# Kernel tuning notes

Measured on AMD Instinct MI355X. Metric: run time of the kernel, lower is better.

The kernel has to match this reference:

```python
import jax, jax.numpy as jnp
import numpy as np

LN_EPS = 1e-3  # keras LayerNormalization default epsilon


def setup_inputs() -> dict:
    key = jax.random.key(0)
    ks = jax.random.split(key, 6)
    B, H, W, C = 8, 64, 64, 256
    s = 1.0 / np.sqrt(C)
    return {
        "x": jax.random.normal(ks[0], (B, H, W, C), jnp.float32),
        "gamma": jnp.ones((C,), jnp.float32),
        "beta": jnp.zeros((C,), jnp.float32),
        "wq": jax.random.normal(ks[1], (C, C), jnp.float32) * s,
        "bq": jnp.zeros((C,), jnp.float32),
        "wk": jax.random.normal(ks[2], (C, C), jnp.float32) * s,
        "bk": jnp.zeros((C,), jnp.float32),
        "wv": jax.random.normal(ks[3], (C, C), jnp.float32) * s,
        "bv": jnp.zeros((C,), jnp.float32),
        "wo": jax.random.normal(ks[4], (C, C), jnp.float32) * s,
        "bo": jnp.zeros((C,), jnp.float32),
    }


def reference(x, gamma, beta, wq, bq, wk, bk, wv, bv, wo, bo):
    B, H, W, C = x.shape
    # LayerNormalization over channel axis (keras default axis=-1, eps=1e-3)
    mean = jnp.mean(x, axis=-1, keepdims=True)
    var = jnp.mean(jnp.square(x - mean), axis=-1, keepdims=True)
    h = (x - mean) * jax.lax.rsqrt(var + LN_EPS) * gamma + beta

    q = h @ wq + bq
    k = h @ wk + bk
    v = h @ wv + bv

    # flatten spatial dims: single-head attention over N = H*W positions
    N = H * W
    qf = q.reshape(B, N, C)
    kf = k.reshape(B, N, C)
    vf = v.reshape(B, N, C)

    scale = jnp.asarray(C, x.dtype) ** -0.5
    scores = jnp.einsum('bnc,bmc->bnm', qf, kf) * scale  # [B, N, N]
    attn = jax.nn.softmax(scores, axis=-1)
    o = jnp.einsum('bnm,bmc->bnc', attn, vf).reshape(B, H, W, C)

    o = o @ wo + bo
    return x + o
```

## Files before the change

### kernel.cpp

```cpp
#include <hip/hip_runtime.h>
#include <hip/hip_bf16.h>
#include <stdint.h>

typedef __attribute__((ext_vector_type(8))) short bf16x8;
typedef __attribute__((ext_vector_type(4))) short s16x4;
typedef __attribute__((ext_vector_type(4))) float f32x4;

__device__ __forceinline__ unsigned short f2b(float x) {
  __hip_bfloat16 h = __float2bfloat16(x);
  unsigned short u;
  __builtin_memcpy(&u, &h, 2);
  return u;
}

__device__ __forceinline__ float b2f(unsigned short u) {
  unsigned v = (unsigned)u << 16;
  float f;
  __builtin_memcpy(&f, &v, 4);
  return f;
}

__device__ __forceinline__ void glds16(const void* g, void* l) {
  __builtin_amdgcn_global_load_lds((const __attribute__((address_space(1))) void*)g,
                                   (__attribute__((address_space(3))) void*)l,
                                   16, 0, 0);
}

__device__ __forceinline__ float wred_add(float v) {
#pragma unroll
  for (int o = 32; o >= 1; o >>= 1) v += __shfl_xor(v, o, 64);
  return v;
}

__global__ __launch_bounds__(256) void gemm_qkv(
    const unsigned short* __restrict__ h, const unsigned short* __restrict__ wT,
    const float* __restrict__ bq, const float* __restrict__ bk, const float* __restrict__ bv,
    unsigned short* __restrict__ q, unsigned short* __restrict__ kk,
    unsigned short* __restrict__ vT, float qscale)
{
  __shared__ unsigned short As[128 * 32];
  __shared__ unsigned short Bs[128 * 32];
  const int t = threadIdx.x;
  const int lane = t & 63;
  const int wv_ = t >> 6;
  const int wr = wv_ >> 1, wc = wv_ & 1;
  const int z = blockIdx.z;
  const long long row0 = (long long)blockIdx.y * 128;
  const int col0 = blockIdx.x * 128;
  const unsigned short* Bt = wT + z * 65536;
  const float* bias = z == 0 ? bq : z == 1 ? bk : bv;
  const float scale = z == 0 ? qscale : 1.0f;

  const int sr = t >> 2;
  const int sc = (t & 3) * 8;
  const unsigned short* ga = h + (row0 + sr) * 256 + sc;
  const unsigned short* gb = Bt + (col0 + sr) * 256 + sc;
  char* lA = (char*)As + (t >> 6) * 1024;
  char* lB = (char*)Bs + (t >> 6) * 1024;

  const int l15 = lane & 15;
  const int l4 = lane >> 4;
  const unsigned short* pa = As + (wr * 64 + l15) * 32 + l4 * 8;
  const unsigned short* pb = Bs + (wc * 64 + l15) * 32 + l4 * 8;

  f32x4 acc[4][4] = {};

  for (int k0 = 0; k0 < 256; k0 += 32) {
    glds16(ga, lA);
    glds16(ga + 64 * 256, lA + 4096);
    glds16(gb, lB);
    glds16(gb + 64 * 256, lB + 4096);
    ga += 32;
    gb += 32;
    __syncthreads();
    bf16x8 a[4], b[4];
#pragma unroll
    for (int i = 0; i < 4; i++) a[i] = *(const bf16x8*)(pa + i * 512);
#pragma unroll
    for (int j = 0; j < 4; j++) b[j] = *(const bf16x8*)(pb + j * 512);
#pragma unroll
    for (int i = 0; i < 4; i++)
#pragma unroll
      for (int j = 0; j < 4; j++)
        acc[i][j] = __builtin_amdgcn_mfma_f32_16x16x32_bf16(a[i], b[j], acc[i][j], 0, 0, 0);
    __syncthreads();
  }

#pragma unroll
  for (int i = 0; i < 4; i++) {
#pragma unroll
    for (int j = 0; j < 4; j++) {
      const int col = col0 + wc * 64 + j * 16 + l15;
      const float bv_ = bias[col];
#pragma unroll
      for (int r = 0; r < 4; r++) {
        const long long row = row0 + wr * 64 + i * 16 + l4 * 4 + r;
        const float val = (acc[i][j][r] + bv_) * scale;
        if (z == 0) {
          q[row * 256 + col] = f2b(val);
        } else if (z == 1) {
          kk[row * 256 + col] = f2b(val);
        } else {
          const int bb = (int)(row >> 12), rr = (int)(row & 4095);
          const int kl = rr & 31;
          const int rrp = (rr & ~31) | ((((kl >> 2) & 3) << 3) | (((kl >> 4) & 1) << 2) | (kl & 3));
          vT[((long long)bb * 256 + col) * 4096 + rrp] = f2b(val);
        }
      }
    }
  }
}

__global__ __launch_bounds__(256) void gemm_out(
    const unsigned short* __restrict__ A, const unsigned short* __restrict__ Bt,
    float* __restrict__ C, const float* __restrict__ bias,
    const float* __restrict__ resid)
{
  __shared__ unsigned short As[128 * 32];
  __shared__ unsigned short Bs[128 * 32];
  const int t = threadIdx.x;
  const int lane = t & 63;
  const int wv_ = t >> 6;
  const int wr = wv_ >> 1, wc = wv_ & 1;
  const long long row0 = (long long)blockIdx.y * 128;
  const int col0 = blockIdx.x * 128;

  const int sr = t >> 2;
  const int sc = (t & 3) * 8;
  const unsigned short* ga = A + (row0 + sr) * 256 + sc;
  const unsigned short* gb = Bt + (col0 + sr) * 256 + sc;
  char* lA = (char*)As + (t >> 6) * 1024;
  char* lB = (char*)Bs + (t >> 6) * 1024;

  const int l15 = lane & 15;
  const int l4 = lane >> 4;
  const unsigned short* pa = As + (wr * 64 + l15) * 32 + l4 * 8;
  const unsigned short* pb = Bs + (wc * 64 + l15) * 32 + l4 * 8;

  f32x4 acc[4][4] = {};

  for (int k0 = 0; k0 < 256; k0 += 32) {
    glds16(ga, lA);
    glds16(ga + 64 * 256, lA + 4096);
    glds16(gb, lB);
    glds16(gb + 64 * 256, lB + 4096);
    ga += 32;
    gb += 32;
    __syncthreads();
    bf16x8 a[4], b[4];
#pragma unroll
    for (int i = 0; i < 4; i++) a[i] = *(const bf16x8*)(pa + i * 512);
#pragma unroll
    for (int j = 0; j < 4; j++) b[j] = *(const bf16x8*)(pb + j * 512);
#pragma unroll
    for (int i = 0; i < 4; i++)
#pragma unroll
      for (int j = 0; j < 4; j++)
        acc[i][j] = __builtin_amdgcn_mfma_f32_16x16x32_bf16(a[i], b[j], acc[i][j], 0, 0, 0);
    __syncthreads();
  }

#pragma unroll
  for (int i = 0; i < 4; i++) {
#pragma unroll
    for (int j = 0; j < 4; j++) {
      const int col = col0 + wc * 64 + j * 16 + l15;
      const float bv_ = bias[col];
#pragma unroll
      for (int r = 0; r < 4; r++) {
        const long long row = row0 + wr * 64 + i * 16 + l4 * 4 + r;
        const long long idx = row * 256 + col;
        C[idx] = resid[idx] + acc[i][j][r] + bv_;
      }
    }
  }
}

__global__ __launch_bounds__(512) void ln_bf16(const float* __restrict__ x,
                                               const float* __restrict__ gamma,
                                               const float* __restrict__ beta,
                                               unsigned short* __restrict__ h)
{
  const int w = threadIdx.x >> 6;
  const int lane = threadIdx.x & 63;
  const long long row = (long long)blockIdx.x * 8 + w;
  const f32x4 v = *(const f32x4*)(x + row * 256 + lane * 4);
  const f32x4 g = *(const f32x4*)(gamma + lane * 4);
  const f32x4 be = *(const f32x4*)(beta + lane * 4);
  float s = v[0] + v[1] + v[2] + v[3];
  float s2 = v[0] * v[0] + v[1] * v[1] + v[2] * v[2] + v[3] * v[3];
#pragma unroll
  for (int o = 32; o >= 1; o >>= 1) {
    s += __shfl_xor(s, o, 64);
    s2 += __shfl_xor(s2, o, 64);
  }
  const float mean = s * (1.f / 256.f);
  const float var = s2 * (1.f / 256.f) - mean * mean;
  const float rstd = rsqrtf(var + 1e-3f);
  s16x4 out;
#pragma unroll
  for (int e = 0; e < 4; e++) out[e] = (short)f2b((v[e] - mean) * rstd * g[e] + be[e]);
  *(s16x4*)(h + row * 256 + lane * 4) = out;
}

__global__ void wtrans(const float* __restrict__ wq, const float* __restrict__ wk,
                       const float* __restrict__ wv, const float* __restrict__ wo,
                       unsigned short* __restrict__ wT)
{
  const float* w = blockIdx.z == 0 ? wq : blockIdx.z == 1 ? wk : blockIdx.z == 2 ? wv : wo;
  unsigned short* o = wT + (long long)blockIdx.z * 65536;
  __shared__ float tile[16][17];
  const int tx = threadIdx.x, ty = threadIdx.y;
  const int bx = blockIdx.x * 16, by = blockIdx.y * 16;
  tile[ty][tx] = w[(by + ty) * 256 + bx + tx];
  __syncthreads();
  o[(bx + ty) * 256 + (by + tx)] = f2b(tile[tx][ty]);
}

#define FL_LDS (64 * 1024)

__global__ __launch_bounds__(256, 2) void flash(
    const unsigned short* __restrict__ q,
    const unsigned short* __restrict__ kk,
    const unsigned short* __restrict__ vT,
    unsigned short* __restrict__ o0,
    unsigned short* __restrict__ o1,
    float2* __restrict__ ml0,
    float2* __restrict__ ml1)
{
  extern __shared__ char lds[];
  const int t = threadIdx.x;
  const int w = t >> 6;
  const int lane = t & 63;
  const int l15 = lane & 15, hi = lane >> 4;
  const int b = blockIdx.x & 7;
  const int kh = (blockIdx.x >> 3) & 1;
  const int qb = blockIdx.x >> 4;
  const long long qrow = (long long)b * 4096 + (long long)qb * 128 + w * 32;

  const unsigned short* kbase = kk + (long long)b * 4096 * 256 + (long long)kh * 2048 * 256;
  const unsigned short* vbase = vT + (long long)b * 256 * 4096 + kh * 2048;

  const int gs_k = (t & 31) ^ ((t >> 5) & 7);
  const unsigned short* Kst = kbase + (t >> 5) * 256 + gs_k * 8;
  const int gs_v = (t & 3) ^ ((t >> 2) & 3);
  const unsigned short* Vst = vbase + (long long)(t >> 2) * 4096 + gs_v * 8;

  bf16x8 Qf[2][8];
#pragma unroll
  for (int qg = 0; qg < 2; qg++) {
    const unsigned short* qp = q + (qrow + qg * 16 + l15) * 256 + hi * 8;
#pragma unroll
    for (int ks = 0; ks < 8; ks++) Qf[qg][ks] = *(const bf16x8*)(qp + ks * 32);
  }

  f32x4 O[2][16] = {};
  float mrow[2] = {-1e30f, -1e30f};
  float lrow[2] = {0.f, 0.f};

  auto stage = [&](int it, int c) {
    const unsigned short* ks_ = Kst + (long long)it * 32 * 256;
    const unsigned short* vs_ = Vst + it * 32;
    char* kd = lds + c * 16384 + w * 1024;
    char* vd = lds + 32768 + c * 16384 + w * 1024;
#pragma unroll
    for (int p = 0; p < 4; p++) {
      glds16(ks_ + p * 8 * 256, kd + p * 4096);
      glds16(vs_ + (long long)p * 64 * 4096, vd + p * 4096);
    }
  };

  stage(0, 0);

  for (int it = 0; it < 64; ++it) {
    const int cur = it & 1;
    __builtin_amdgcn_s_barrier();
    if (it < 63) {
      stage(it + 1, cur ^ 1);
      asm volatile("s_waitcnt vmcnt(8)" ::: "memory");
    } else {
      asm volatile("s_waitcnt vmcnt(0)" ::: "memory");
    }
    __builtin_amdgcn_sched_barrier(0);
    __builtin_amdgcn_s_barrier();
    const char* Kb = lds + cur * 16384;
    const char* Vb = lds + 32768 + cur * 16384;

    f32x4 S[2][2] = {};
    __builtin_amdgcn_s_setprio(1);
#pragma unroll
    for (int ks = 0; ks < 8; ks++) {
#pragma unroll
      for (int j = 0; j < 2; j++) {
        bf16x8 Kf = *(const bf16x8*)(Kb + (j * 16 + l15) * 512 +
                                     ((ks * 64 + hi * 16) ^ ((l15 & 7) << 4)));
        S[0][j] = __builtin_amdgcn_mfma_f32_16x16x32_bf16(Kf, Qf[0][ks], S[0][j], 0, 0, 0);
        S[1][j] = __builtin_amdgcn_mfma_f32_16x16x32_bf16(Kf, Qf[1][ks], S[1][j], 0, 0, 0);
      }
    }
    __builtin_amdgcn_s_setprio(0);

    bf16x8 Pf8[2];
#pragma unroll
    for (int qg = 0; qg < 2; qg++) {
      float mx = fmaxf(fmaxf(fmaxf(S[qg][0][0], S[qg][0][1]), fmaxf(S[qg][0][2], S[qg][0][3])),
                       fmaxf(fmaxf(S[qg][1][0], S[qg][1][1]), fmaxf(S[qg][1][2], S[qg][1][3])));
      mx = fmaxf(mx, __shfl_xor(mx, 16, 64));
      mx = fmaxf(mx, __shfl_xor(mx, 32, 64));
      if (!__all(mx <= mrow[qg] + 8.f)) {
        const float mn = fmaxf(mrow[qg], mx);
        const float rs_ = exp2f(mrow[qg] - mn);
        mrow[qg] = mn;
        lrow[qg] *= rs_;
#pragma unroll
        for (int dg = 0; dg < 16; dg++) O[qg][dg] *= rs_;
      }
      float sum = 0.f;
      float e[2][4];
#pragma unroll
      for (int j = 0; j < 2; j++)
#pragma unroll
        for (int r = 0; r < 4; r++) {
          e[j][r] = exp2f(S[qg][j][r] - mrow[qg]);
          sum += e[j][r];
        }
      sum += __shfl_xor(sum, 16, 64);
      sum += __shfl_xor(sum, 32, 64);
      lrow[qg] += sum;
      bf16x8 p;
#pragma unroll
      for (int j = 0; j < 2; j++)
#pragma unroll
        for (int r = 0; r < 4; r++) p[j * 4 + r] = (short)f2b(e[j][r]);
      Pf8[qg] = p;
    }

    __builtin_amdgcn_s_setprio(1);
#pragma unroll
    for (int dg = 0; dg < 16; dg++) {
      bf16x8 Vf8 = *(const bf16x8*)(Vb + (dg * 16 + l15) * 64 +
                                    ((hi * 16) ^ ((l15 & 3) << 4)));
      O[0][dg] = __builtin_amdgcn_mfma_f32_16x16x32_bf16(Vf8, Pf8[0], O[0][dg], 0, 0, 0);
      O[1][dg] = __builtin_amdgcn_mfma_f32_16x16x32_bf16(Vf8, Pf8[1], O[1][dg], 0, 0, 0);
    }
    __builtin_amdgcn_s_setprio(0);
  }

  unsigned short* const op = kh ? o1 : o0;
  float2* const mlp = kh ? ml1 : ml0;
  __syncthreads();
  char* const slab = lds + w * 16384;
#pragma unroll
  for (int qg = 0; qg < 2; qg++) {
#pragma unroll
    for (int dg = 0; dg < 16; dg++) {
      f32x4 v = O[qg][dg];
      *(f32x4*)(slab + l15 * 1024 + ((dg * 64 + hi * 16) ^ ((l15 & 7) << 4))) = v;
    }
    if (hi == 0) mlp[qrow + qg * 16 + l15] = make_float2(mrow[qg], lrow[qg]);
    const int qq = lane >> 2;
    const int dc = lane & 3;
    const long long orow = (qrow + qg * 16 + qq) * 256 + dc * 64;
#pragma unroll
    for (int half = 0; half < 8; half++) {
      bf16x8 pack;
#pragma unroll
      for (int di = 0; di < 2; di++) {
        f32x4 v = *(const f32x4*)(slab + qq * 1024 +
                                  ((dc * 256 + half * 32 + di * 16) ^ ((qq & 7) << 4)));
#pragma unroll
        for (int e2 = 0; e2 < 4; e2++) pack[di * 4 + e2] = (short)f2b(v[e2]);
      }
      *(bf16x8*)(op + orow + half * 8) = pack;
    }
    __syncthreads();
  }
}

__global__ __launch_bounds__(256) void merge_halves(
    unsigned short* __restrict__ o0, const unsigned short* __restrict__ o1,
    const float2* __restrict__ ml0, const float2* __restrict__ ml1)
{
  const int t = threadIdx.x;
  const long long row = (long long)blockIdx.x * 8 + (t >> 5);
  const int ch = t & 31;
  const float2 a = ml0[row];
  const float2 c = ml1[row];
  const float M = fmaxf(a.x, c.x);
  const float w0 = exp2f(a.x - M);
  const float w1 = exp2f(c.x - M);
  const float inv = 1.f / (w0 * a.y + w1 * c.y);
  const long long idx = row * 256 + ch * 8;
  bf16x8 u0 = *(const bf16x8*)(o0 + idx);
  bf16x8 u1 = *(const bf16x8*)(o1 + idx);
  bf16x8 out;
#pragma unroll
  for (int e = 0; e < 8; e++) {
    const float v = (w0 * b2f((unsigned short)u0[e]) + w1 * b2f((unsigned short)u1[e])) * inv;
    out[e] = (short)f2b(v);
  }
  *(bf16x8*)(o0 + idx) = out;
}

extern "C" void kernel_launch(void* const* d_in, const int* in_sizes, int n_in,
                              void* d_out, int out_size, void* d_ws, size_t ws_size,
                              hipStream_t stream)
{
  const float* x = (const float*)d_in[0];
  const float* gamma = (const float*)d_in[1];
  const float* beta = (const float*)d_in[2];
  const float* wq = (const float*)d_in[3];
  const float* bq = (const float*)d_in[4];
  const float* wk = (const float*)d_in[5];
  const float* bk = (const float*)d_in[6];
  const float* wv = (const float*)d_in[7];
  const float* bv = (const float*)d_in[8];
  const float* wo = (const float*)d_in[9];
  const float* bo = (const float*)d_in[10];

  const int Cc = 256;
  const long long MR = 32768;

  char* base = (char*)d_ws;
  size_t off = 0;
  auto take = [&](size_t bytes) -> char* {
    char* p = base + off;
    off = (off + bytes + 255) & ~(size_t)255;
    return p;
  };
  unsigned short* h   = (unsigned short*)take((size_t)MR * Cc * 2);
  unsigned short* q   = (unsigned short*)take((size_t)MR * Cc * 2);
  unsigned short* kk  = (unsigned short*)take((size_t)MR * Cc * 2);
  unsigned short* vT  = (unsigned short*)take((size_t)MR * Cc * 2);
  unsigned short* oo  = (unsigned short*)take((size_t)MR * Cc * 2);
  unsigned short* o1  = (unsigned short*)take((size_t)MR * Cc * 2);
  unsigned short* wT  = (unsigned short*)take(4ull * Cc * Cc * 2);
  float2* ml0 = (float2*)take((size_t)MR * sizeof(float2));
  float2* ml1 = (float2*)take((size_t)MR * sizeof(float2));

  wtrans<<<dim3(16, 16, 4), dim3(16, 16), 0, stream>>>(wq, wk, wv, wo, wT);
  ln_bf16<<<dim3((unsigned)(MR / 8)), dim3(512), 0, stream>>>(x, gamma, beta, h);

  const float qscale = 0.0625f * 1.44269504f;
  gemm_qkv<<<dim3(2, 256, 3), 256, 0, stream>>>(h, wT, bq, bk, bv, q, kk, vT, qscale);

  flash<<<dim3(512), dim3(256), FL_LDS, stream>>>(q, kk, vT, oo, o1, ml0, ml1);
  merge_halves<<<dim3((unsigned)(MR / 8)), dim3(256), 0, stream>>>(oo, o1, ml0, ml1);

  gemm_out<<<dim3(2, 256, 1), 256, 0, stream>>>(oo, wT + 3 * 65536, (float*)d_out, bo, x);
}
```

Before: 252.2 us.

## Fuse split-KV merge into output GEMM and defer row-sum reductions

Removes the separate merge_halves kernel: gemm_out now loads both partial attention outputs plus their max/sum stats, computes the combine weights per row, and writes the merged bf16 A tile into LDS itself instead of using async global-to-LDS loads. Inside the flash loop, the per-iteration cross-lane reductions for the row sum are dropped and done once at the end, and the max shuffle runs only when the rescale branch triggers. This saves one kernel launch, a full read-write pass over the output, and some per-tile shuffles. The cost is that gemm_out reads twice the A data through registers, and skipping the max reduction can leave lanes with different running maxima, which is only safe because of the per-lane threshold check.

```diff
diff --git a/kernel.cpp b/kernel.cpp
--- a/kernel.cpp
+++ b/kernel.cpp
@@ -24,12 +24,6 @@
   __builtin_amdgcn_global_load_lds((const __attribute__((address_space(1))) void*)g,
                                    (__attribute__((address_space(3))) void*)l,
                                    16, 0, 0);
-}
-
-__device__ __forceinline__ float wred_add(float v) {
-#pragma unroll
-  for (int o = 32; o >= 1; o >>= 1) v += __shfl_xor(v, o, 64);
-  return v;
 }
 
 __global__ __launch_bounds__(256) void gemm_qkv(
@@ -112,7 +106,9 @@
 }
 
 __global__ __launch_bounds__(256) void gemm_out(
-    const unsigned short* __restrict__ A, const unsigned short* __restrict__ Bt,
+    const unsigned short* __restrict__ o0, const unsigned short* __restrict__ o1,
+    const float2* __restrict__ ml0, const float2* __restrict__ ml1,
+    const unsigned short* __restrict__ Bt,
     float* __restrict__ C, const float* __restrict__ bias,
     const float* __restrict__ resid)
 {
@@ -127,9 +123,27 @@
 
   const int sr = t >> 2;
   const int sc = (t & 3) * 8;
-  const unsigned short* ga = A + (row0 + sr) * 256 + sc;
+  const long long ar0 = row0 + sr;
+  float f0a, f1a, f0b, f1b;
+  {
+    const float2 a = ml0[ar0], c = ml1[ar0];
+    const float M = fmaxf(a.x, c.x);
+    const float w0 = exp2f(a.x - M), w1 = exp2f(c.x - M);
+    const float inv = 1.f / (w0 * a.y + w1 * c.y);
+    f0a = w0 * inv;
+    f1a = w1 * inv;
+  }
+  {
+    const float2 a = ml0[ar0 + 64], c = ml1[ar0 + 64];
+    const float M = fmaxf(a.x, c.x);
+    const float w0 = exp2f(a.x - M), w1 = exp2f(c.x - M);
+    const float inv = 1.f / (w0 * a.y + w1 * c.y);
+    f0b = w0 * inv;
+    f1b = w1 * inv;
+  }
+  const unsigned short* g0 = o0 + ar0 * 256 + sc;
+  const unsigned short* g1 = o1 + ar0 * 256 + sc;
   const unsigned short* gb = Bt + (col0 + sr) * 256 + sc;
-  char* lA = (char*)As + (t >> 6) * 1024;
   char* lB = (char*)Bs + (t >> 6) * 1024;
 
   const int l15 = lane & 15;
@@ -140,11 +154,22 @@
   f32x4 acc[4][4] = {};
 
   for (int k0 = 0; k0 < 256; k0 += 32) {
-    glds16(ga, lA);
-    glds16(ga + 64 * 256, lA + 4096);
+    bf16x8 u0 = *(const bf16x8*)g0;
+    bf16x8 u1 = *(const bf16x8*)g1;
+    bf16x8 v0 = *(const bf16x8*)(g0 + 64 * 256);
+    bf16x8 v1 = *(const bf16x8*)(g1 + 64 * 256);
+    bf16x8 m0, m1;
+#pragma unroll
+    for (int e = 0; e < 8; e++) {
+      m0[e] = (short)f2b(f0a * b2f((unsigned short)u0[e]) + f1a * b2f((unsigned short)u1[e]));
+      m1[e] = (short)f2b(f0b * b2f((unsigned short)v0[e]) + f1b * b2f((unsigned short)v1[e]));
+    }
+    *(bf16x8*)((char*)As + t * 16) = m0;
+    *(bf16x8*)((char*)As + 4096 + t * 16) = m1;
     glds16(gb, lB);
     glds16(gb + 64 * 256, lB + 4096);
-    ga += 32;
+    g0 += 32;
+    g1 += 32;
     gb += 32;
     __syncthreads();
     bf16x8 a[4], b[4];
@@ -303,11 +328,12 @@
     bf16x8 Pf8[2];
 #pragma unroll
     for (int qg = 0; qg < 2; qg++) {
-      float mx = fmaxf(fmaxf(fmaxf(S[qg][0][0], S[qg][0][1]), fmaxf(S[qg][0][2], S[qg][0][3])),
-                       fmaxf(fmaxf(S[qg][1][0], S[qg][1][1]), fmaxf(S[qg][1][2], S[qg][1][3])));
-      mx = fmaxf(mx, __shfl_xor(mx, 16, 64));
-      mx = fmaxf(mx, __shfl_xor(mx, 32, 64));
-      if (!__all(mx <= mrow[qg] + 8.f)) {
+      const float mxl =
+          fmaxf(fmaxf(fmaxf(S[qg][0][0], S[qg][0][1]), fmaxf(S[qg][0][2], S[qg][0][3])),
+                fmaxf(fmaxf(S[qg][1][0], S[qg][1][1]), fmaxf(S[qg][1][2], S[qg][1][3])));
+      if (!__all(mxl <= mrow[qg] + 8.f)) {
+        float mx = fmaxf(mxl, __shfl_xor(mxl, 16, 64));
+        mx = fmaxf(mx, __shfl_xor(mx, 32, 64));
         const float mn = fmaxf(mrow[qg], mx);
         const float rs_ = exp2f(mrow[qg] - mn);
         mrow[qg] = mn;
@@ -324,8 +350,6 @@
           e[j][r] = exp2f(S[qg][j][r] - mrow[qg]);
           sum += e[j][r];
         }
-      sum += __shfl_xor(sum, 16, 64);
-      sum += __shfl_xor(sum, 32, 64);
       lrow[qg] += sum;
       bf16x8 p;
 #pragma unroll
@@ -352,12 +376,15 @@
   char* const slab = lds + w * 16384;
 #pragma unroll
   for (int qg = 0; qg < 2; qg++) {
+    float lr = lrow[qg];
+    lr += __shfl_xor(lr, 16, 64);
+    lr += __shfl_xor(lr, 32, 64);
 #pragma unroll
     for (int dg = 0; dg < 16; dg++) {
       f32x4 v = O[qg][dg];
       *(f32x4*)(slab + l15 * 1024 + ((dg * 64 + hi * 16) ^ ((l15 & 7) << 4))) = v;
     }
-    if (hi == 0) mlp[qrow + qg * 16 + l15] = make_float2(mrow[qg], lrow[qg]);
+    if (hi == 0) mlp[qrow + qg * 16 + l15] = make_float2(mrow[qg], lr);
     const int qq = lane >> 2;
     const int dc = lane & 3;
     const long long orow = (qrow + qg * 16 + qq) * 256 + dc * 64;
@@ -375,31 +402,6 @@
     }
     __syncthreads();
   }
-}
-
-__global__ __launch_bounds__(256) void merge_halves(
-    unsigned short* __restrict__ o0, const unsigned short* __restrict__ o1,
-    const float2* __restrict__ ml0, const float2* __restrict__ ml1)
-{
-  const int t = threadIdx.x;
-  const long long row = (long long)blockIdx.x * 8 + (t >> 5);
-  const int ch = t & 31;
-  const float2 a = ml0[row];
-  const float2 c = ml1[row];
-  const float M = fmaxf(a.x, c.x);
-  const float w0 = exp2f(a.x - M);
-  const float w1 = exp2f(c.x - M);
-  const float inv = 1.f / (w0 * a.y + w1 * c.y);
-  const long long idx = row * 256 + ch * 8;
-  bf16x8 u0 = *(const bf16x8*)(o0 + idx);
-  bf16x8 u1 = *(const bf16x8*)(o1 + idx);
-  bf16x8 out;
-#pragma unroll
-  for (int e = 0; e < 8; e++) {
-    const float v = (w0 * b2f((unsigned short)u0[e]) + w1 * b2f((unsigned short)u1[e])) * inv;
-    out[e] = (short)f2b(v);
-  }
-  *(bf16x8*)(o0 + idx) = out;
 }
 
 extern "C" void kernel_launch(void* const* d_in, const int* in_sizes, int n_in,
@@ -432,7 +434,7 @@
   unsigned short* q   = (unsigned short*)take((size_t)MR * Cc * 2);
   unsigned short* kk  = (unsigned short*)take((size_t)MR * Cc * 2);
   unsigned short* vT  = (unsigned short*)take((size_t)MR * Cc * 2);
-  unsigned short* oo  = (unsigned short*)take((size_t)MR * Cc * 2);
+  unsigned short* o0  = (unsigned short*)take((size_t)MR * Cc * 2);
   unsigned short* o1  = (unsigned short*)take((size_t)MR * Cc * 2);
   unsigned short* wT  = (unsigned short*)take(4ull * Cc * Cc * 2);
   float2* ml0 = (float2*)take((size_t)MR * sizeof(float2));
@@ -444,8 +446,8 @@
   const float qscale = 0.0625f * 1.44269504f;
   gemm_qkv<<<dim3(2, 256, 3), 256, 0, stream>>>(h, wT, bq, bk, bv, q, kk, vT, qscale);
 
-  flash<<<dim3(512), dim3(256), FL_LDS, stream>>>(q, kk, vT, oo, o1, ml0, ml1);
-  merge_halves<<<dim3((unsigned)(MR / 8)), dim3(256), 0, stream>>>(oo, o1, ml0, ml1);
-
-  gemm_out<<<dim3(2, 256, 1), 256, 0, stream>>>(oo, wT + 3 * 65536, (float*)d_out, bo, x);
-}
+  flash<<<dim3(512), dim3(256), FL_LDS, stream>>>(q, kk, vT, o0, o1, ml0, ml1);
+
+  gemm_out<<<dim3(2, 256, 1), 256, 0, stream>>>(o0, o1, ml0, ml1, wT + 3 * 65536,
+                                                (float*)d_out, bo, x);
+}
```

After: 228.4 us. 1.1x faster.
